# Optimization experiments

Hardware: AMD Instinct MI355X
Metric: run time of the kernel (lower is better)

## Reference

```python
import math
import jax, jax.numpy as jnp
import numpy as np

B, Q, K, D, H, C = 4, 1024, 1024, 256, 8, 32  # batch, q_len, kv_len, model dim, heads, per-head dim


def setup_inputs() -> dict:
    key = jax.random.key(0)
    ks = jax.random.split(key, 9)
    s = 1.0 / math.sqrt(D)
    return {
        "q_x": jax.random.normal(ks[0], (B, Q, D), jnp.float32),
        "kv_x": jax.random.normal(ks[1], (B, K, D), jnp.float32),
        "bias_mask": jax.random.normal(ks[2], (B, 1, 1, K), jnp.float32),
        "bias_pair": jax.random.normal(ks[3], (B, H, Q, K), jnp.float32),
        "wq": jax.random.normal(ks[4], (D, H * C), jnp.float32) * s,
        "wk": jax.random.normal(ks[5], (D, H * C), jnp.float32) * s,
        "wv": jax.random.normal(ks[6], (D, H * C), jnp.float32) * s,
        "wg": jnp.zeros((D, H * C), jnp.float32),  # gating init: weights 0
        "bg": jnp.ones((H * C,), jnp.float32),     # gating init: bias 1
        "wo": jax.random.normal(ks[7], (H * C, D), jnp.float32) * s,
        "bo": jnp.zeros((D,), jnp.float32),
    }


def reference(q_x, kv_x, bias_mask, bias_pair, wq, wk, wv, wg, bg, wo, bo):
    # project and split heads: [B, L, H, C]
    q = (q_x @ wq).reshape(B, Q, H, C) / math.sqrt(C)
    k = (kv_x @ wk).reshape(B, K, H, C)
    v = (kv_x @ wv).reshape(B, K, H, C)
    # scores [B, H, Q, K] with multiple additive biases
    scores = jnp.einsum("bqhc,bkhc->bhqk", q, k) + bias_mask + bias_pair
    a = jax.nn.softmax(scores, axis=-1)
    o = jnp.einsum("bhqk,bkhc->bqhc", a, v).reshape(B, Q, H * C)
    # sigmoid gate from query activations
    g = jax.nn.sigmoid(q_x @ wg + bg)
    o = o * g
    return o @ wo + bo
```

## Files before the change

kernel.cpp:

```cpp
#include <hip/hip_runtime.h>
#include <hip/hip_bf16.h>


typedef short bf16x8 __attribute__((ext_vector_type(8)));
typedef float f32x4 __attribute__((ext_vector_type(4)));

__device__ __forceinline__ unsigned short f2bf(float f) {
  __hip_bfloat16 hb = __float2bfloat16(f);
  return *reinterpret_cast<const unsigned short*>(&hb);
}

__global__ __launch_bounds__(256) void transpose_conv(
    const float* __restrict__ wq, const float* __restrict__ wk,
    const float* __restrict__ wv, const float* __restrict__ wg,
    const float* __restrict__ wo, unsigned short* __restrict__ wt) {
  __shared__ float t[64][65];
  const int widx = blockIdx.x >> 4;
  const int tile = blockIdx.x & 15;
  const float* src = widx == 0 ? wq : widx == 1 ? wk
                     : widx == 2 ? wv : widx == 3 ? wg : wo;
  unsigned short* dst = wt + widx * 65536;
  const int r0 = (tile >> 2) * 64, c0 = (tile & 3) * 64;
  const int tr = threadIdx.x >> 4;
  const int tc4 = (threadIdx.x & 15) * 4;
#pragma unroll
  for (int i = 0; i < 4; ++i) {
    const float4 u = *reinterpret_cast<const float4*>(
        src + (size_t)(r0 + tr + i * 16) * 256 + c0 + tc4);
    t[tr + i * 16][tc4 + 0] = u.x;
    t[tr + i * 16][tc4 + 1] = u.y;
    t[tr + i * 16][tc4 + 2] = u.z;
    t[tr + i * 16][tc4 + 3] = u.w;
  }
  __syncthreads();
#pragma unroll
  for (int i = 0; i < 4; ++i) {
    const int rr = tr + i * 16;
    ushort4 o;
    o.x = f2bf(t[tc4 + 0][rr]);
    o.y = f2bf(t[tc4 + 1][rr]);
    o.z = f2bf(t[tc4 + 2][rr]);
    o.w = f2bf(t[tc4 + 3][rr]);
    *reinterpret_cast<ushort4*>(dst + (size_t)(c0 + rr) * 256 + r0 + tc4) = o;
  }
}

__global__ __launch_bounds__(256) void proj_mfma(
    const float* __restrict__ q_x, const float* __restrict__ kv_x,
    const unsigned short* __restrict__ wt, const float* __restrict__ bg,
    unsigned short* __restrict__ qhb, unsigned short* __restrict__ khb,
    unsigned short* __restrict__ vhb, float* __restrict__ gws) {
  const int side = blockIdx.y;
  const int m0 = blockIdx.x * 16;
  const int lane = threadIdx.x & 63;
  const int n0 = (threadIdx.x >> 6) * 64;
  const int mrow = lane & 15;
  const int quad = lane >> 4;
  const float* X = side ? kv_x : q_x;
  const unsigned short* W0 = wt + (side ? 1 : 0) * 65536;
  const unsigned short* W1 = wt + (side ? 2 : 3) * 65536;
  f32x4 acc0[4], acc1[4];
  const f32x4 z = {0.f, 0.f, 0.f, 0.f};
#pragma unroll
  for (int nt = 0; nt < 4; ++nt) { acc0[nt] = z; acc1[nt] = z; }

  for (int k0 = 0; k0 < 256; k0 += 32) {
    const size_t abase = (size_t)(m0 + mrow) * 256 + k0 + quad * 8;
    const float4 a0 = *reinterpret_cast<const float4*>(X + abase);
    const float4 a1 = *reinterpret_cast<const float4*>(X + abase + 4);
    bf16x8 a;
    a[0] = (short)f2bf(a0.x); a[1] = (short)f2bf(a0.y);
    a[2] = (short)f2bf(a0.z); a[3] = (short)f2bf(a0.w);
    a[4] = (short)f2bf(a1.x); a[5] = (short)f2bf(a1.y);
    a[6] = (short)f2bf(a1.z); a[7] = (short)f2bf(a1.w);
#pragma unroll
    for (int nt = 0; nt < 4; ++nt) {
      const size_t wrow = (size_t)(n0 + nt * 16 + mrow) * 256 + k0 + quad * 8;
      const bf16x8 b0 = *reinterpret_cast<const bf16x8*>(W0 + wrow);
      const bf16x8 b1 = *reinterpret_cast<const bf16x8*>(W1 + wrow);
      acc0[nt] = __builtin_amdgcn_mfma_f32_16x16x32_bf16(a, b0, acc0[nt], 0, 0, 0);
      acc1[nt] = __builtin_amdgcn_mfma_f32_16x16x32_bf16(a, b1, acc1[nt], 0, 0, 0);
    }
  }

  const int b = m0 >> 10;
#pragma unroll
  for (int nt = 0; nt < 4; ++nt) {
    const int n = n0 + nt * 16 + mrow;
    const int h = n >> 5, c = n & 31;
    const float bgv = (side == 0) ? bg[n] : 0.f;
#pragma unroll
    for (int r = 0; r < 4; ++r) {
      const int row = m0 + quad * 4 + r;
      const int qp = row & 1023;
      const size_t o = ((size_t)(b * 8 + h) * 1024 + qp) * 32 + c;
      if (side == 0) {
        qhb[o] = f2bf(acc0[nt][r] * 0.17677669529663689f);
        const float zz = acc1[nt][r] + bgv;
        gws[(size_t)row * 256 + n] = 1.0f / (1.0f + __expf(-zz));
      } else {
        khb[o] = f2bf(acc0[nt][r]);
        vhb[o] = f2bf(acc1[nt][r]);
      }
    }
  }
}

__global__ __launch_bounds__(256) void attn_mfma(
    const unsigned short* __restrict__ qhb,
    const unsigned short* __restrict__ khb,
    const unsigned short* __restrict__ vhb,
    const float* __restrict__ bias_mask,
    const float* __restrict__ bias_pair,
    const float* __restrict__ gws, unsigned short* __restrict__ og) {
  __shared__ unsigned short ks[2][64 * 40];
  __shared__ unsigned short vsT[2][32 * 72];
  __shared__ unsigned short ps[64 * 72];
  const int x = blockIdx.x;
  const int b = x >> 7, h = (x >> 4) & 7, q0 = (x & 15) * 64;
  const int tid = threadIdx.x;
  const int wv = tid >> 6, lane = tid & 63, quad = lane >> 4, lr = lane & 15;
  const int bh = b * 8 + h;

  const bf16x8 aq = *reinterpret_cast<const bf16x8*>(
      qhb + ((size_t)bh * 1024 + q0 + wv * 16 + lr) * 32 + quad * 8);

  float m[4], l[4];
  f32x4 oa[2];
  const f32x4 zero4 = {0.f, 0.f, 0.f, 0.f};
  oa[0] = zero4; oa[1] = zero4;
#pragma unroll
  for (int r = 0; r < 4; ++r) { m[r] = -3e30f; l[r] = 0.f; }

  const float* bp = bias_pair + ((size_t)bh * 1024 + q0 + wv * 16) * 1024;
  const float* bm = bias_mask + (size_t)b * 1024;
  const unsigned short* kbase = khb + (size_t)bh * 32768;
  const unsigned short* vbase = vhb + (size_t)bh * 32768;
  const int srow = tid >> 2, sc8 = (tid & 3) * 8;

  {
    const bf16x8 k0v = *reinterpret_cast<const bf16x8*>(kbase + srow * 32 + sc8);
    const bf16x8 v0v = *reinterpret_cast<const bf16x8*>(vbase + srow * 32 + sc8);
    *reinterpret_cast<bf16x8*>(&ks[0][srow * 40 + sc8]) = k0v;
#pragma unroll
    for (int i = 0; i < 8; ++i)
      vsT[0][(sc8 + i) * 72 + srow] = (unsigned short)v0v[i];
  }
  float bpr[4][4], mkr[4];
#pragma unroll
  for (int nt = 0; nt < 4; ++nt) {
    mkr[nt] = bm[16 * nt + lr];
#pragma unroll
    for (int r = 0; r < 4; ++r)
      bpr[nt][r] = bp[(size_t)(quad * 4 + r) * 1024 + 16 * nt + lr];
  }
  __syncthreads();

  for (int kt = 0; kt < 16; ++kt) {
    const int cur = kt & 1;

    bf16x8 kn, vn;
    float bpn[4][4], mkn[4];
    if (kt < 15) {
      const int kk1 = (kt + 1) * 64;
      kn = *reinterpret_cast<const bf16x8*>(kbase + (size_t)(kk1 + srow) * 32 + sc8);
      vn = *reinterpret_cast<const bf16x8*>(vbase + (size_t)(kk1 + srow) * 32 + sc8);
#pragma unroll
      for (int nt = 0; nt < 4; ++nt) {
        mkn[nt] = bm[kk1 + 16 * nt + lr];
#pragma unroll
        for (int r = 0; r < 4; ++r)
          bpn[nt][r] = bp[(size_t)(quad * 4 + r) * 1024 + kk1 + 16 * nt + lr];
      }
    }

    f32x4 s[4];
#pragma unroll
    for (int nt = 0; nt < 4; ++nt) {
#pragma unroll
      for (int r = 0; r < 4; ++r) s[nt][r] = bpr[nt][r] + mkr[nt];
      const bf16x8 bk = *reinterpret_cast<const bf16x8*>(
          &ks[cur][(16 * nt + lr) * 40 + quad * 8]);
      s[nt] = __builtin_amdgcn_mfma_f32_16x16x32_bf16(aq, bk, s[nt], 0, 0, 0);
    }

#pragma unroll
    for (int r = 0; r < 4; ++r) {
      float mx = fmaxf(fmaxf(s[0][r], s[1][r]), fmaxf(s[2][r], s[3][r]));
      mx = fmaxf(mx, __shfl_xor(mx, 1));
      mx = fmaxf(mx, __shfl_xor(mx, 2));
      mx = fmaxf(mx, __shfl_xor(mx, 4));
      mx = fmaxf(mx, __shfl_xor(mx, 8));
      const float mn = fmaxf(m[r], mx);
      const float alpha = __expf(m[r] - mn);
      float rs = 0.f;
#pragma unroll
      for (int nt = 0; nt < 4; ++nt) {
        s[nt][r] = __expf(s[nt][r] - mn);
        rs += s[nt][r];
      }
      rs += __shfl_xor(rs, 1);
      rs += __shfl_xor(rs, 2);
      rs += __shfl_xor(rs, 4);
      rs += __shfl_xor(rs, 8);
      l[r] = l[r] * alpha + rs;
      m[r] = mn;
      oa[0][r] *= alpha;
      oa[1][r] *= alpha;
      const int ri = wv * 16 + quad * 4 + r;
#pragma unroll
      for (int nt = 0; nt < 4; ++nt)
        ps[ri * 72 + 16 * nt + lr] = f2bf(s[nt][r]);
    }
    asm volatile("s_waitcnt lgkmcnt(0)" ::: "memory");

#pragma unroll
    for (int k0i = 0; k0i < 2; ++k0i) {
      const bf16x8 ap = *reinterpret_cast<const bf16x8*>(
          &ps[(wv * 16 + lr) * 72 + k0i * 32 + quad * 8]);
#pragma unroll
      for (int nt2 = 0; nt2 < 2; ++nt2) {
        const bf16x8 bv = *reinterpret_cast<const bf16x8*>(
            &vsT[cur][(nt2 * 16 + lr) * 72 + k0i * 32 + quad * 8]);
        oa[nt2] = __builtin_amdgcn_mfma_f32_16x16x32_bf16(ap, bv, oa[nt2], 0, 0, 0);
      }
    }

    if (kt < 15) {
      *reinterpret_cast<bf16x8*>(&ks[cur ^ 1][srow * 40 + sc8]) = kn;
#pragma unroll
      for (int i = 0; i < 8; ++i)
        vsT[cur ^ 1][(sc8 + i) * 72 + srow] = (unsigned short)vn[i];
#pragma unroll
      for (int nt = 0; nt < 4; ++nt) {
        mkr[nt] = mkn[nt];
#pragma unroll
        for (int r = 0; r < 4; ++r) bpr[nt][r] = bpn[nt][r];
      }
    }
    __syncthreads();
  }

#pragma unroll
  for (int r = 0; r < 4; ++r) {
    const int qr = q0 + wv * 16 + quad * 4 + r;
    const float inv = 1.0f / l[r];
    const size_t base = ((size_t)b * 1024 + qr) * 256 + h * 32;
#pragma unroll
    for (int nt2 = 0; nt2 < 2; ++nt2) {
      const int c = nt2 * 16 + lr;
      og[base + c] = f2bf(oa[nt2][r] * inv * gws[base + c]);
    }
  }
}

__global__ __launch_bounds__(256) void outproj_mfma(
    const unsigned short* __restrict__ og,
    const unsigned short* __restrict__ wt,
    const float* __restrict__ bo, float* __restrict__ out) {
  const int m0 = blockIdx.x * 16;
  const int lane = threadIdx.x & 63;
  const int n0 = (threadIdx.x >> 6) * 64;
  const int mrow = lane & 15;
  const int quad = lane >> 4;
  const unsigned short* W = wt + 4 * 65536;
  f32x4 acc[4];
  const f32x4 z = {0.f, 0.f, 0.f, 0.f};
#pragma unroll
  for (int nt = 0; nt < 4; ++nt) acc[nt] = z;

  for (int k0 = 0; k0 < 256; k0 += 32) {
    const bf16x8 a = *reinterpret_cast<const bf16x8*>(
        og + (size_t)(m0 + mrow) * 256 + k0 + quad * 8);
#pragma unroll
    for (int nt = 0; nt < 4; ++nt) {
      const bf16x8 b = *reinterpret_cast<const bf16x8*>(
          W + (size_t)(n0 + nt * 16 + mrow) * 256 + k0 + quad * 8);
      acc[nt] = __builtin_amdgcn_mfma_f32_16x16x32_bf16(a, b, acc[nt], 0, 0, 0);
    }
  }

#pragma unroll
  for (int nt = 0; nt < 4; ++nt) {
    const int n = n0 + nt * 16 + mrow;
    const float bov = bo[n];
#pragma unroll
    for (int r = 0; r < 4; ++r) {
      const int row = m0 + quad * 4 + r;
      out[(size_t)row * 256 + n] = acc[nt][r] + bov;
    }
  }
}

extern "C" void kernel_launch(void* const* d_in, const int* in_sizes, int n_in,
                              void* d_out, int out_size, void* d_ws,
                              size_t ws_size, hipStream_t stream) {
  (void)in_sizes; (void)n_in; (void)out_size; (void)ws_size;
  const float* q_x = (const float*)d_in[0];
  const float* kv_x = (const float*)d_in[1];
  const float* bias_mask = (const float*)d_in[2];
  const float* bias_pair = (const float*)d_in[3];
  const float* wq = (const float*)d_in[4];
  const float* wk = (const float*)d_in[5];
  const float* wv = (const float*)d_in[6];
  const float* wg = (const float*)d_in[7];
  const float* bg = (const float*)d_in[8];
  const float* wo = (const float*)d_in[9];
  const float* bo = (const float*)d_in[10];

  char* wsb = (char*)d_ws;
  unsigned short* wt  = (unsigned short*)(wsb);
  unsigned short* qhb = (unsigned short*)(wsb + 655360);
  unsigned short* khb = (unsigned short*)(wsb + 2752512);
  unsigned short* vhb = (unsigned short*)(wsb + 4849664);
  unsigned short* og  = (unsigned short*)(wsb + 6946816);
  float* gws          = (float*)(wsb + 9043968);

  transpose_conv<<<80, 256, 0, stream>>>(wq, wk, wv, wg, wo, wt);
  proj_mfma<<<dim3(256, 2), 256, 0, stream>>>(q_x, kv_x, wt, bg, qhb, khb,
                                              vhb, gws);
  attn_mfma<<<512, 256, 0, stream>>>(qhb, khb, vhb, bias_mask, bias_pair, gws,
                                     og);
  outproj_mfma<<<256, 256, 0, stream>>>(og, wt, bo, (float*)d_out);
}
```

Baseline: 255.3 us.

## Fuse all stages into one persistent kernel with software grid barriers

Measured after the change: 405.5 us. +58.8%, slower.

```diff
diff --git a/kernel.cpp b/kernel.cpp
--- a/kernel.cpp
+++ b/kernel.cpp
@@ -10,284 +10,299 @@
   return *reinterpret_cast<const unsigned short*>(&hb);
 }
 
-__global__ __launch_bounds__(256) void transpose_conv(
+__device__ __forceinline__ void gridbar(unsigned* ctr, unsigned nb) {
+  __syncthreads();
+  if (threadIdx.x == 0) {
+    __threadfence();
+    atomicAdd(ctr, 1u);
+    while (atomicAdd(ctr, 0u) < nb) __builtin_amdgcn_s_sleep(2);
+    __threadfence();
+  }
+  __syncthreads();
+}
+
+__global__ void bar_init(unsigned* ctrs) {
+  if (threadIdx.x < 3) ctrs[threadIdx.x] = 0u;
+}
+
+__global__ __launch_bounds__(256, 2) void fused_all(
+    const float* __restrict__ q_x, const float* __restrict__ kv_x,
+    const float* __restrict__ bias_mask, const float* __restrict__ bias_pair,
     const float* __restrict__ wq, const float* __restrict__ wk,
     const float* __restrict__ wv, const float* __restrict__ wg,
-    const float* __restrict__ wo, unsigned short* __restrict__ wt) {
+    const float* __restrict__ bg, const float* __restrict__ wo,
+    const float* __restrict__ bo, float* __restrict__ out,
+    unsigned short* __restrict__ wt, unsigned short* __restrict__ qhb,
+    unsigned short* __restrict__ khb, unsigned short* __restrict__ vhb,
+    unsigned short* __restrict__ og, float* __restrict__ gws,
+    unsigned* __restrict__ bars) {
   __shared__ float t[64][65];
-  const int widx = blockIdx.x >> 4;
-  const int tile = blockIdx.x & 15;
-  const float* src = widx == 0 ? wq : widx == 1 ? wk
-                     : widx == 2 ? wv : widx == 3 ? wg : wo;
-  unsigned short* dst = wt + widx * 65536;
-  const int r0 = (tile >> 2) * 64, c0 = (tile & 3) * 64;
-  const int tr = threadIdx.x >> 4;
-  const int tc4 = (threadIdx.x & 15) * 4;
-#pragma unroll
-  for (int i = 0; i < 4; ++i) {
-    const float4 u = *reinterpret_cast<const float4*>(
-        src + (size_t)(r0 + tr + i * 16) * 256 + c0 + tc4);
-    t[tr + i * 16][tc4 + 0] = u.x;
-    t[tr + i * 16][tc4 + 1] = u.y;
-    t[tr + i * 16][tc4 + 2] = u.z;
-    t[tr + i * 16][tc4 + 3] = u.w;
-  }
-  __syncthreads();
-#pragma unroll
-  for (int i = 0; i < 4; ++i) {
-    const int rr = tr + i * 16;
-    ushort4 o;
-    o.x = f2bf(t[tc4 + 0][rr]);
-    o.y = f2bf(t[tc4 + 1][rr]);
-    o.z = f2bf(t[tc4 + 2][rr]);
-    o.w = f2bf(t[tc4 + 3][rr]);
-    *reinterpret_cast<ushort4*>(dst + (size_t)(c0 + rr) * 256 + r0 + tc4) = o;
-  }
-}
-
-__global__ __launch_bounds__(256) void proj_mfma(
-    const float* __restrict__ q_x, const float* __restrict__ kv_x,
-    const unsigned short* __restrict__ wt, const float* __restrict__ bg,
-    unsigned short* __restrict__ qhb, unsigned short* __restrict__ khb,
-    unsigned short* __restrict__ vhb, float* __restrict__ gws) {
-  const int side = blockIdx.y;
-  const int m0 = blockIdx.x * 16;
-  const int lane = threadIdx.x & 63;
-  const int n0 = (threadIdx.x >> 6) * 64;
-  const int mrow = lane & 15;
-  const int quad = lane >> 4;
-  const float* X = side ? kv_x : q_x;
-  const unsigned short* W0 = wt + (side ? 1 : 0) * 65536;
-  const unsigned short* W1 = wt + (side ? 2 : 3) * 65536;
-  f32x4 acc0[4], acc1[4];
-  const f32x4 z = {0.f, 0.f, 0.f, 0.f};
-#pragma unroll
-  for (int nt = 0; nt < 4; ++nt) { acc0[nt] = z; acc1[nt] = z; }
-
-  for (int k0 = 0; k0 < 256; k0 += 32) {
-    const size_t abase = (size_t)(m0 + mrow) * 256 + k0 + quad * 8;
-    const float4 a0 = *reinterpret_cast<const float4*>(X + abase);
-    const float4 a1 = *reinterpret_cast<const float4*>(X + abase + 4);
-    bf16x8 a;
-    a[0] = (short)f2bf(a0.x); a[1] = (short)f2bf(a0.y);
-    a[2] = (short)f2bf(a0.z); a[3] = (short)f2bf(a0.w);
-    a[4] = (short)f2bf(a1.x); a[5] = (short)f2bf(a1.y);
-    a[6] = (short)f2bf(a1.z); a[7] = (short)f2bf(a1.w);
-#pragma unroll
-    for (int nt = 0; nt < 4; ++nt) {
-      const size_t wrow = (size_t)(n0 + nt * 16 + mrow) * 256 + k0 + quad * 8;
-      const bf16x8 b0 = *reinterpret_cast<const bf16x8*>(W0 + wrow);
-      const bf16x8 b1 = *reinterpret_cast<const bf16x8*>(W1 + wrow);
-      acc0[nt] = __builtin_amdgcn_mfma_f32_16x16x32_bf16(a, b0, acc0[nt], 0, 0, 0);
-      acc1[nt] = __builtin_amdgcn_mfma_f32_16x16x32_bf16(a, b1, acc1[nt], 0, 0, 0);
-    }
-  }
-
-  const int b = m0 >> 10;
-#pragma unroll
-  for (int nt = 0; nt < 4; ++nt) {
-    const int n = n0 + nt * 16 + mrow;
-    const int h = n >> 5, c = n & 31;
-    const float bgv = (side == 0) ? bg[n] : 0.f;
-#pragma unroll
-    for (int r = 0; r < 4; ++r) {
-      const int row = m0 + quad * 4 + r;
-      const int qp = row & 1023;
-      const size_t o = ((size_t)(b * 8 + h) * 1024 + qp) * 32 + c;
-      if (side == 0) {
-        qhb[o] = f2bf(acc0[nt][r] * 0.17677669529663689f);
-        const float zz = acc1[nt][r] + bgv;
-        gws[(size_t)row * 256 + n] = 1.0f / (1.0f + __expf(-zz));
-      } else {
-        khb[o] = f2bf(acc0[nt][r]);
-        vhb[o] = f2bf(acc1[nt][r]);
-      }
-    }
-  }
-}
-
-__global__ __launch_bounds__(256) void attn_mfma(
-    const unsigned short* __restrict__ qhb,
-    const unsigned short* __restrict__ khb,
-    const unsigned short* __restrict__ vhb,
-    const float* __restrict__ bias_mask,
-    const float* __restrict__ bias_pair,
-    const float* __restrict__ gws, unsigned short* __restrict__ og) {
   __shared__ unsigned short ks[2][64 * 40];
   __shared__ unsigned short vsT[2][32 * 72];
   __shared__ unsigned short ps[64 * 72];
-  const int x = blockIdx.x;
-  const int b = x >> 7, h = (x >> 4) & 7, q0 = (x & 15) * 64;
+
+  const int bid = blockIdx.x;
   const int tid = threadIdx.x;
-  const int wv = tid >> 6, lane = tid & 63, quad = lane >> 4, lr = lane & 15;
-  const int bh = b * 8 + h;
-
-  const bf16x8 aq = *reinterpret_cast<const bf16x8*>(
-      qhb + ((size_t)bh * 1024 + q0 + wv * 16 + lr) * 32 + quad * 8);
-
-  float m[4], l[4];
-  f32x4 oa[2];
-  const f32x4 zero4 = {0.f, 0.f, 0.f, 0.f};
-  oa[0] = zero4; oa[1] = zero4;
-#pragma unroll
-  for (int r = 0; r < 4; ++r) { m[r] = -3e30f; l[r] = 0.f; }
-
-  const float* bp = bias_pair + ((size_t)bh * 1024 + q0 + wv * 16) * 1024;
-  const float* bm = bias_mask + (size_t)b * 1024;
-  const unsigned short* kbase = khb + (size_t)bh * 32768;
-  const unsigned short* vbase = vhb + (size_t)bh * 32768;
-  const int srow = tid >> 2, sc8 = (tid & 3) * 8;
+  const int lane = tid & 63;
+  const int quad = lane >> 4;
+  const int lr = lane & 15;
+  const int mrow = lane & 15;
+
+  if (bid < 80) {
+    const int widx = bid >> 4;
+    const int tile = bid & 15;
+    const float* src = widx == 0 ? wq : widx == 1 ? wk
+                       : widx == 2 ? wv : widx == 3 ? wg : wo;
+    unsigned short* dst = wt + widx * 65536;
+    const int r0 = (tile >> 2) * 64, c0 = (tile & 3) * 64;
+    const int tr = tid >> 4;
+    const int tc4 = (tid & 15) * 4;
+#pragma unroll
+    for (int i = 0; i < 4; ++i) {
+      const float4 u = *reinterpret_cast<const float4*>(
+          src + (size_t)(r0 + tr + i * 16) * 256 + c0 + tc4);
+      t[tr + i * 16][tc4 + 0] = u.x;
+      t[tr + i * 16][tc4 + 1] = u.y;
+      t[tr + i * 16][tc4 + 2] = u.z;
+      t[tr + i * 16][tc4 + 3] = u.w;
+    }
+    __syncthreads();
+#pragma unroll
+    for (int i = 0; i < 4; ++i) {
+      const int rr = tr + i * 16;
+      ushort4 o;
+      o.x = f2bf(t[tc4 + 0][rr]);
+      o.y = f2bf(t[tc4 + 1][rr]);
+      o.z = f2bf(t[tc4 + 2][rr]);
+      o.w = f2bf(t[tc4 + 3][rr]);
+      *reinterpret_cast<ushort4*>(dst + (size_t)(c0 + rr) * 256 + r0 + tc4) = o;
+    }
+  }
+  gridbar(&bars[0], 512u);
 
   {
-    const bf16x8 k0v = *reinterpret_cast<const bf16x8*>(kbase + srow * 32 + sc8);
-    const bf16x8 v0v = *reinterpret_cast<const bf16x8*>(vbase + srow * 32 + sc8);
-    *reinterpret_cast<bf16x8*>(&ks[0][srow * 40 + sc8]) = k0v;
-#pragma unroll
-    for (int i = 0; i < 8; ++i)
-      vsT[0][(sc8 + i) * 72 + srow] = (unsigned short)v0v[i];
-  }
-  float bpr[4][4], mkr[4];
-#pragma unroll
-  for (int nt = 0; nt < 4; ++nt) {
-    mkr[nt] = bm[16 * nt + lr];
-#pragma unroll
-    for (int r = 0; r < 4; ++r)
-      bpr[nt][r] = bp[(size_t)(quad * 4 + r) * 1024 + 16 * nt + lr];
-  }
-  __syncthreads();
-
-  for (int kt = 0; kt < 16; ++kt) {
-    const int cur = kt & 1;
-
-    bf16x8 kn, vn;
-    float bpn[4][4], mkn[4];
-    if (kt < 15) {
-      const int kk1 = (kt + 1) * 64;
-      kn = *reinterpret_cast<const bf16x8*>(kbase + (size_t)(kk1 + srow) * 32 + sc8);
-      vn = *reinterpret_cast<const bf16x8*>(vbase + (size_t)(kk1 + srow) * 32 + sc8);
+    const int side = bid >> 8;
+    const int m0 = (bid & 255) * 16;
+    const int n0 = (tid >> 6) * 64;
+    const float* X = side ? kv_x : q_x;
+    const unsigned short* W0 = wt + (side ? 1 : 0) * 65536;
+    const unsigned short* W1 = wt + (side ? 2 : 3) * 65536;
+    f32x4 acc0[4], acc1[4];
+    const f32x4 z = {0.f, 0.f, 0.f, 0.f};
+#pragma unroll
+    for (int nt = 0; nt < 4; ++nt) { acc0[nt] = z; acc1[nt] = z; }
+
+    for (int k0 = 0; k0 < 256; k0 += 32) {
+      const size_t abase = (size_t)(m0 + mrow) * 256 + k0 + quad * 8;
+      const float4 a0 = *reinterpret_cast<const float4*>(X + abase);
+      const float4 a1 = *reinterpret_cast<const float4*>(X + abase + 4);
+      bf16x8 a;
+      a[0] = (short)f2bf(a0.x); a[1] = (short)f2bf(a0.y);
+      a[2] = (short)f2bf(a0.z); a[3] = (short)f2bf(a0.w);
+      a[4] = (short)f2bf(a1.x); a[5] = (short)f2bf(a1.y);
+      a[6] = (short)f2bf(a1.z); a[7] = (short)f2bf(a1.w);
 #pragma unroll
       for (int nt = 0; nt < 4; ++nt) {
-        mkn[nt] = bm[kk1 + 16 * nt + lr];
-#pragma unroll
-        for (int r = 0; r < 4; ++r)
-          bpn[nt][r] = bp[(size_t)(quad * 4 + r) * 1024 + kk1 + 16 * nt + lr];
-      }
-    }
-
-    f32x4 s[4];
+        const size_t wrow = (size_t)(n0 + nt * 16 + mrow) * 256 + k0 + quad * 8;
+        const bf16x8 b0 = *reinterpret_cast<const bf16x8*>(W0 + wrow);
+        const bf16x8 b1 = *reinterpret_cast<const bf16x8*>(W1 + wrow);
+        acc0[nt] = __builtin_amdgcn_mfma_f32_16x16x32_bf16(a, b0, acc0[nt], 0, 0, 0);
+        acc1[nt] = __builtin_amdgcn_mfma_f32_16x16x32_bf16(a, b1, acc1[nt], 0, 0, 0);
+      }
+    }
+
+    const int b = m0 >> 10;
 #pragma unroll
     for (int nt = 0; nt < 4; ++nt) {
-#pragma unroll
-      for (int r = 0; r < 4; ++r) s[nt][r] = bpr[nt][r] + mkr[nt];
-      const bf16x8 bk = *reinterpret_cast<const bf16x8*>(
-          &ks[cur][(16 * nt + lr) * 40 + quad * 8]);
-      s[nt] = __builtin_amdgcn_mfma_f32_16x16x32_bf16(aq, bk, s[nt], 0, 0, 0);
+      const int n = n0 + nt * 16 + mrow;
+      const int h = n >> 5, c = n & 31;
+      const float bgv = (side == 0) ? bg[n] : 0.f;
+#pragma unroll
+      for (int r = 0; r < 4; ++r) {
+        const int row = m0 + quad * 4 + r;
+        const int qp = row & 1023;
+        const size_t o = ((size_t)(b * 8 + h) * 1024 + qp) * 32 + c;
+        if (side == 0) {
+          qhb[o] = f2bf(acc0[nt][r] * 0.17677669529663689f);
+          const float zz = acc1[nt][r] + bgv;
+          gws[(size_t)row * 256 + n] = 1.0f / (1.0f + __expf(-zz));
+        } else {
+          khb[o] = f2bf(acc0[nt][r]);
+          vhb[o] = f2bf(acc1[nt][r]);
+        }
+      }
+    }
+  }
+  gridbar(&bars[1], 512u);
+
+  {
+    const int b = bid >> 7, h = (bid >> 4) & 7, q0 = (bid & 15) * 64;
+    const int wv4 = tid >> 6;
+    const int bh = b * 8 + h;
+
+    const bf16x8 aq = *reinterpret_cast<const bf16x8*>(
+        qhb + ((size_t)bh * 1024 + q0 + wv4 * 16 + lr) * 32 + quad * 8);
+
+    float m[4], l[4];
+    f32x4 oa[2];
+    const f32x4 zero4 = {0.f, 0.f, 0.f, 0.f};
+    oa[0] = zero4; oa[1] = zero4;
+#pragma unroll
+    for (int r = 0; r < 4; ++r) { m[r] = -3e30f; l[r] = 0.f; }
+
+    const float* bp = bias_pair + ((size_t)bh * 1024 + q0 + wv4 * 16) * 1024;
+    const float* bm = bias_mask + (size_t)b * 1024;
+    const unsigned short* kbase = khb + (size_t)bh * 32768;
+    const unsigned short* vbase = vhb + (size_t)bh * 32768;
+    const int srow = tid >> 2, sc8 = (tid & 3) * 8;
+
+    {
+      const bf16x8 k0v = *reinterpret_cast<const bf16x8*>(kbase + srow * 32 + sc8);
+      const bf16x8 v0v = *reinterpret_cast<const bf16x8*>(vbase + srow * 32 + sc8);
+      *reinterpret_cast<bf16x8*>(&ks[0][srow * 40 + sc8]) = k0v;
+#pragma unroll
+      for (int i = 0; i < 8; ++i)
+        vsT[0][(sc8 + i) * 72 + srow] = (unsigned short)v0v[i];
+    }
+    float bpr[4][4], mkr[4];
+#pragma unroll
+    for (int nt = 0; nt < 4; ++nt) {
+      mkr[nt] = bm[16 * nt + lr];
+#pragma unroll
+      for (int r = 0; r < 4; ++r)
+        bpr[nt][r] = bp[(size_t)(quad * 4 + r) * 1024 + 16 * nt + lr];
+    }
+    __syncthreads();
+
+    for (int kt = 0; kt < 16; ++kt) {
+      const int cur = kt & 1;
+
+      bf16x8 kn, vn;
+      float bpn[4][4], mkn[4];
+      if (kt < 15) {
+        const int kk1 = (kt + 1) * 64;
+        kn = *reinterpret_cast<const bf16x8*>(kbase + (size_t)(kk1 + srow) * 32 + sc8);
+        vn = *reinterpret_cast<const bf16x8*>(vbase + (size_t)(kk1 + srow) * 32 + sc8);
+#pragma unroll
+        for (int nt = 0; nt < 4; ++nt) {
+          mkn[nt] = bm[kk1 + 16 * nt + lr];
+#pragma unroll
+          for (int r = 0; r < 4; ++r)
+            bpn[nt][r] = bp[(size_t)(quad * 4 + r) * 1024 + kk1 + 16 * nt + lr];
+        }
+      }
+
+      f32x4 s[4];
+#pragma unroll
+      for (int nt = 0; nt < 4; ++nt) {
+#pragma unroll
+        for (int r = 0; r < 4; ++r) s[nt][r] = bpr[nt][r] + mkr[nt];
+        const bf16x8 bk = *reinterpret_cast<const bf16x8*>(
+            &ks[cur][(16 * nt + lr) * 40 + quad * 8]);
+        s[nt] = __builtin_amdgcn_mfma_f32_16x16x32_bf16(aq, bk, s[nt], 0, 0, 0);
+      }
+
+#pragma unroll
+      for (int r = 0; r < 4; ++r) {
+        float mx = fmaxf(fmaxf(s[0][r], s[1][r]), fmaxf(s[2][r], s[3][r]));
+        mx = fmaxf(mx, __shfl_xor(mx, 1));
+        mx = fmaxf(mx, __shfl_xor(mx, 2));
+        mx = fmaxf(mx, __shfl_xor(mx, 4));
+        mx = fmaxf(mx, __shfl_xor(mx, 8));
+        const float mn = fmaxf(m[r], mx);
+        const float alpha = __expf(m[r] - mn);
+        float rs = 0.f;
+#pragma unroll
+        for (int nt = 0; nt < 4; ++nt) {
+          s[nt][r] = __expf(s[nt][r] - mn);
+          rs += s[nt][r];
+        }
+        rs += __shfl_xor(rs, 1);
+        rs += __shfl_xor(rs, 2);
+        rs += __shfl_xor(rs, 4);
+        rs += __shfl_xor(rs, 8);
+        l[r] = l[r] * alpha + rs;
+        m[r] = mn;
+        oa[0][r] *= alpha;
+        oa[1][r] *= alpha;
+        const int ri = wv4 * 16 + quad * 4 + r;
+#pragma unroll
+        for (int nt = 0; nt < 4; ++nt)
+          ps[ri * 72 + 16 * nt + lr] = f2bf(s[nt][r]);
+      }
+      asm volatile("s_waitcnt lgkmcnt(0)" ::: "memory");
+
+#pragma unroll
+      for (int k0i = 0; k0i < 2; ++k0i) {
+        const bf16x8 ap = *reinterpret_cast<const bf16x8*>(
+            &ps[(wv4 * 16 + lr) * 72 + k0i * 32 + quad * 8]);
+#pragma unroll
+        for (int nt2 = 0; nt2 < 2; ++nt2) {
+          const bf16x8 bv = *reinterpret_cast<const bf16x8*>(
+              &vsT[cur][(nt2 * 16 + lr) * 72 + k0i * 32 + quad * 8]);
+          oa[nt2] = __builtin_amdgcn_mfma_f32_16x16x32_bf16(ap, bv, oa[nt2], 0, 0, 0);
+        }
+      }
+
+      if (kt < 15) {
+        *reinterpret_cast<bf16x8*>(&ks[cur ^ 1][srow * 40 + sc8]) = kn;
+#pragma unroll
+        for (int i = 0; i < 8; ++i)
+          vsT[cur ^ 1][(sc8 + i) * 72 + srow] = (unsigned short)vn[i];
+#pragma unroll
+        for (int nt = 0; nt < 4; ++nt) {
+          mkr[nt] = mkn[nt];
+#pragma unroll
+          for (int r = 0; r < 4; ++r) bpr[nt][r] = bpn[nt][r];
+        }
+      }
+      __syncthreads();
     }
 
 #pragma unroll
     for (int r = 0; r < 4; ++r) {
-      float mx = fmaxf(fmaxf(s[0][r], s[1][r]), fmaxf(s[2][r], s[3][r]));
-      mx = fmaxf(mx, __shfl_xor(mx, 1));
-      mx = fmaxf(mx, __shfl_xor(mx, 2));
-      mx = fmaxf(mx, __shfl_xor(mx, 4));
-      mx = fmaxf(mx, __shfl_xor(mx, 8));
-      const float mn = fmaxf(m[r], mx);
-      const float alpha = __expf(m[r] - mn);
-      float rs = 0.f;
-#pragma unroll
-      for (int nt = 0; nt < 4; ++nt) {
-        s[nt][r] = __expf(s[nt][r] - mn);
-        rs += s[nt][r];
-      }
-      rs += __shfl_xor(rs, 1);
-      rs += __shfl_xor(rs, 2);
-      rs += __shfl_xor(rs, 4);
-      rs += __shfl_xor(rs, 8);
-      l[r] = l[r] * alpha + rs;
-      m[r] = mn;
-      oa[0][r] *= alpha;
-      oa[1][r] *= alpha;
-      const int ri = wv * 16 + quad * 4 + r;
-#pragma unroll
-      for (int nt = 0; nt < 4; ++nt)
-        ps[ri * 72 + 16 * nt + lr] = f2bf(s[nt][r]);
-    }
-    asm volatile("s_waitcnt lgkmcnt(0)" ::: "memory");
-
-#pragma unroll
-    for (int k0i = 0; k0i < 2; ++k0i) {
-      const bf16x8 ap = *reinterpret_cast<const bf16x8*>(
-          &ps[(wv * 16 + lr) * 72 + k0i * 32 + quad * 8]);
+      const int qr = q0 + wv4 * 16 + quad * 4 + r;
+      const float inv = 1.0f / l[r];
+      const size_t base = ((size_t)b * 1024 + qr) * 256 + h * 32;
 #pragma unroll
       for (int nt2 = 0; nt2 < 2; ++nt2) {
-        const bf16x8 bv = *reinterpret_cast<const bf16x8*>(
-            &vsT[cur][(nt2 * 16 + lr) * 72 + k0i * 32 + quad * 8]);
-        oa[nt2] = __builtin_amdgcn_mfma_f32_16x16x32_bf16(ap, bv, oa[nt2], 0, 0, 0);
-      }
-    }
-
-    if (kt < 15) {
-      *reinterpret_cast<bf16x8*>(&ks[cur ^ 1][srow * 40 + sc8]) = kn;
-#pragma unroll
-      for (int i = 0; i < 8; ++i)
-        vsT[cur ^ 1][(sc8 + i) * 72 + srow] = (unsigned short)vn[i];
-#pragma unroll
-      for (int nt = 0; nt < 4; ++nt) {
-        mkr[nt] = mkn[nt];
-#pragma unroll
-        for (int r = 0; r < 4; ++r) bpr[nt][r] = bpn[nt][r];
-      }
-    }
-    __syncthreads();
-  }
-
-#pragma unroll
-  for (int r = 0; r < 4; ++r) {
-    const int qr = q0 + wv * 16 + quad * 4 + r;
-    const float inv = 1.0f / l[r];
-    const size_t base = ((size_t)b * 1024 + qr) * 256 + h * 32;
-#pragma unroll
-    for (int nt2 = 0; nt2 < 2; ++nt2) {
-      const int c = nt2 * 16 + lr;
-      og[base + c] = f2bf(oa[nt2][r] * inv * gws[base + c]);
-    }
-  }
-}
-
-__global__ __launch_bounds__(256) void outproj_mfma(
-    const unsigned short* __restrict__ og,
-    const unsigned short* __restrict__ wt,
-    const float* __restrict__ bo, float* __restrict__ out) {
-  const int m0 = blockIdx.x * 16;
-  const int lane = threadIdx.x & 63;
-  const int n0 = (threadIdx.x >> 6) * 64;
-  const int mrow = lane & 15;
-  const int quad = lane >> 4;
-  const unsigned short* W = wt + 4 * 65536;
-  f32x4 acc[4];
-  const f32x4 z = {0.f, 0.f, 0.f, 0.f};
-#pragma unroll
-  for (int nt = 0; nt < 4; ++nt) acc[nt] = z;
-
-  for (int k0 = 0; k0 < 256; k0 += 32) {
-    const bf16x8 a = *reinterpret_cast<const bf16x8*>(
-        og + (size_t)(m0 + mrow) * 256 + k0 + quad * 8);
-#pragma unroll
-    for (int nt = 0; nt < 4; ++nt) {
-      const bf16x8 b = *reinterpret_cast<const bf16x8*>(
-          W + (size_t)(n0 + nt * 16 + mrow) * 256 + k0 + quad * 8);
-      acc[nt] = __builtin_amdgcn_mfma_f32_16x16x32_bf16(a, b, acc[nt], 0, 0, 0);
-    }
-  }
-
-#pragma unroll
-  for (int nt = 0; nt < 4; ++nt) {
-    const int n = n0 + nt * 16 + mrow;
-    const float bov = bo[n];
-#pragma unroll
-    for (int r = 0; r < 4; ++r) {
-      const int row = m0 + quad * 4 + r;
-      out[(size_t)row * 256 + n] = acc[nt][r] + bov;
+        const int c = nt2 * 16 + lr;
+        og[base + c] = f2bf(oa[nt2][r] * inv * gws[base + c]);
+      }
+    }
+  }
+  gridbar(&bars[2], 512u);
+
+  {
+    const int m0 = (bid & 255) * 16;
+    const int nhalf = bid >> 8;
+    const int n0 = nhalf * 128 + (tid >> 6) * 32;
+    const unsigned short* W = wt + 4 * 65536;
+    f32x4 acc[2];
+    const f32x4 z = {0.f, 0.f, 0.f, 0.f};
+    acc[0] = z; acc[1] = z;
+
+#pragma unroll
+    for (int k0 = 0; k0 < 256; k0 += 32) {
+      const bf16x8 a = *reinterpret_cast<const bf16x8*>(
+          og + (size_t)(m0 + mrow) * 256 + k0 + quad * 8);
+#pragma unroll
+      for (int nt = 0; nt < 2; ++nt) {
+        const bf16x8 b = *reinterpret_cast<const bf16x8*>(
+            W + (size_t)(n0 + nt * 16 + mrow) * 256 + k0 + quad * 8);
+        acc[nt] = __builtin_amdgcn_mfma_f32_16x16x32_bf16(a, b, acc[nt], 0, 0, 0);
+      }
+    }
+
+#pragma unroll
+    for (int nt = 0; nt < 2; ++nt) {
+      const int n = n0 + nt * 16 + mrow;
+      const float bov = bo[n];
+#pragma unroll
+      for (int r = 0; r < 4; ++r) {
+        const int row = m0 + quad * 4 + r;
+        out[(size_t)row * 256 + n] = acc[nt][r] + bov;
+      }
     }
   }
 }
@@ -307,6 +322,7 @@
   const float* bg = (const float*)d_in[8];
   const float* wo = (const float*)d_in[9];
   const float* bo = (const float*)d_in[10];
+  float* out = (float*)d_out;
 
   char* wsb = (char*)d_ws;
   unsigned short* wt  = (unsigned short*)(wsb);
@@ -315,11 +331,10 @@
   unsigned short* vhb = (unsigned short*)(wsb + 4849664);
   unsigned short* og  = (unsigned short*)(wsb + 6946816);
   float* gws          = (float*)(wsb + 9043968);
-
-  transpose_conv<<<80, 256, 0, stream>>>(wq, wk, wv, wg, wo, wt);
-  proj_mfma<<<dim3(256, 2), 256, 0, stream>>>(q_x, kv_x, wt, bg, qhb, khb,
-                                              vhb, gws);
-  attn_mfma<<<512, 256, 0, stream>>>(qhb, khb, vhb, bias_mask, bias_pair, gws,
-                                     og);
-  outproj_mfma<<<256, 256, 0, stream>>>(og, wt, bo, (float*)d_out);
-}
+  unsigned* bars      = (unsigned*)(wsb + 13238272);
+
+  bar_init<<<1, 64, 0, stream>>>(bars);
+  fused_all<<<512, 256, 0, stream>>>(
+      q_x, kv_x, bias_mask, bias_pair, wq, wk, wv, wg, bg, wo, bo, out,
+      wt, qhb, khb, vhb, og, gws, bars);
+}
```
